# Optimization experiments

Measured on AMD Instinct MI355X. Metric: run time of the kernel, lower is better.

Reference implementation:

```python
import jax, jax.numpy as jnp
import numpy as np


def setup_inputs() -> dict:
    key = jax.random.key(0)
    k1, k2 = jax.random.split(key)
    N, C, H, W = 64, 1024, 28, 28
    x = jax.random.normal(k1, (N, C, H, W), dtype=jnp.float32)
    fc_weights = jax.random.normal(k2, (C,), dtype=jnp.float32)
    mu = jnp.float32(0.7)
    return {"x": x, "fc_weights": fc_weights, "mu": mu}


def reference(x, fc_weights, mu):
    # cams = relu(x * w_c), shape [N, C, H, W]
    cams = jax.nn.relu(x * fc_weights.reshape(1, -1, 1, 1))
    # per-(sample, channel) spatial max -> threshold
    cam_max = jnp.max(cams, axis=(2, 3), keepdims=True)        # [N, C, 1, 1]
    thr = cam_max * mu
    # drop (zero out) high-activation regions, keep the rest
    dropped = jnp.where(cams > thr, jnp.zeros_like(cams), cams)
    # accumulate over channels -> [N, 1, H, W]
    mean_drop_cam = jnp.sum(dropped, axis=1, keepdims=True)
    return x * mean_drop_cam
```

## Files before the change

### kernel.cpp

```cpp
#include <hip/hip_runtime.h>

#define HWD 784
#define Q4  196
#define CD  1024
#define ND  64

#define CHPB 32
#define NCHUNK (CD / CHPB)

typedef float f32x4 __attribute__((ext_vector_type(4)));

__device__ __forceinline__ float4 cam4(float4 v, float wc) {
    float4 r;
    r.x = fmaxf(v.x * wc, 0.f);
    r.y = fmaxf(v.y * wc, 0.f);
    r.z = fmaxf(v.z * wc, 0.f);
    r.w = fmaxf(v.w * wc, 0.f);
    return r;
}
__device__ __forceinline__ float max4(float4 v) {
    return fmaxf(fmaxf(v.x, v.y), fmaxf(v.z, v.w));
}
__device__ __forceinline__ void accdrop(float4& a, float4 c, float thr) {
    a.x += (c.x > thr) ? 0.f : c.x;
    a.y += (c.y > thr) ? 0.f : c.y;
    a.z += (c.z > thr) ? 0.f : c.z;
    a.w += (c.w > thr) ? 0.f : c.w;
}

__global__ void __launch_bounds__(256) pass1_kernel(const float* __restrict__ x,
                                                    const float* __restrict__ w,
                                                    const float* __restrict__ mu_p,
                                                    float* __restrict__ Spart) {
    __shared__ float4 drp[4][197];

    const int t = threadIdx.x;
    const int wave = t >> 6;
    const int lane = t & 63;
    const int n = blockIdx.y;
    const int cbase = blockIdx.x * CHPB + wave * 8;
    const float mu = mu_p[0];

    const float4* rows = reinterpret_cast<const float4*>(x + ((size_t)n * CD + cbase) * HWD);

    float4 acc0 = {0.f,0.f,0.f,0.f}, acc1 = {0.f,0.f,0.f,0.f};
    float4 acc2 = {0.f,0.f,0.f,0.f}, acc3 = {0.f,0.f,0.f,0.f};

    #pragma unroll 1
    for (int j = 0; j < 8; ++j) {
        const float4* r = rows + j * Q4;
        float4 v0 = r[lane];
        float4 v1 = r[lane + 64];
        float4 v2 = r[lane + 128];
        float4 v3 = (lane < 4) ? r[192 + lane] : float4{0.f,0.f,0.f,0.f};
        const float wc = w[cbase + j];

        v0 = cam4(v0, wc); v1 = cam4(v1, wc); v2 = cam4(v2, wc); v3 = cam4(v3, wc);

        float m = fmaxf(fmaxf(max4(v0), max4(v1)), fmaxf(max4(v2), max4(v3)));
        #pragma unroll
        for (int off = 32; off > 0; off >>= 1)
            m = fmaxf(m, __shfl_xor(m, off, 64));
        const float thr = m * mu;

        accdrop(acc0, v0, thr);
        accdrop(acc1, v1, thr);
        accdrop(acc2, v2, thr);
        accdrop(acc3, v3, thr);
    }

    drp[wave][lane]       = acc0;
    drp[wave][64 + lane]  = acc1;
    drp[wave][128 + lane] = acc2;
    if (lane < 4) drp[wave][192 + lane] = acc3;
    __syncthreads();

    const float* f = reinterpret_cast<const float*>(&drp[0][0]);
    float* sp = Spart + ((size_t)blockIdx.x * ND + n) * HWD;
    for (int p = t; p < HWD; p += 256)
        sp[p] = f[p] + f[788 + p] + f[2 * 788 + p] + f[3 * 788 + p];
}

__global__ void __launch_bounds__(256) reduce_kernel(const float* __restrict__ Spart,
                                                     float* __restrict__ S) {
    const int j = blockIdx.x * 256 + threadIdx.x;
    float s = 0.f;
    #pragma unroll
    for (int ch = 0; ch < NCHUNK; ++ch)
        s += Spart[(size_t)ch * ND * HWD + j];
    S[j] = s;
}

__global__ void __launch_bounds__(256) mult_kernel(const float* __restrict__ x,
                                                   const float* __restrict__ S,
                                                   float* __restrict__ out) {
    const float4* x4 = reinterpret_cast<const float4*>(x);
    const float4* S4 = reinterpret_cast<const float4*>(S);

    const int tid = blockIdx.x * 256 + threadIdx.x;
    const int n   = tid / (64 * Q4);
    const int rem = tid - n * (64 * Q4);
    const int c0  = rem / Q4;
    const int p4  = rem - c0 * Q4;

    const float4 sv = S4[n * Q4 + p4];
    size_t i4 = ((size_t)(n * CD + c0)) * Q4 + p4;

    #pragma unroll 4
    for (int k = 0; k < 16; ++k, i4 += (size_t)64 * Q4) {
        float4 xv = x4[i4];
        float4 o;
        o.x = xv.x * sv.x;
        o.y = xv.y * sv.y;
        o.z = xv.z * sv.z;
        o.w = xv.w * sv.w;
        __builtin_nontemporal_store(*reinterpret_cast<const f32x4*>(&o),
                                    reinterpret_cast<f32x4*>(out) + i4);
    }
}

extern "C" void kernel_launch(void* const* d_in, const int* in_sizes, int n_in,
                              void* d_out, int out_size, void* d_ws, size_t ws_size,
                              hipStream_t stream) {
    const float* x  = (const float*)d_in[0];
    const float* w  = (const float*)d_in[1];
    const float* mu = (const float*)d_in[2];
    float* out = (float*)d_out;

    float* Spart = (float*)d_ws;
    float* S     = Spart + (size_t)NCHUNK * ND * HWD;

    dim3 g1(NCHUNK, ND);
    pass1_kernel<<<g1, 256, 0, stream>>>(x, w, mu, Spart);

    reduce_kernel<<<ND * HWD / 256, 256, 0, stream>>>(Spart, S);

    mult_kernel<<<3136, 256, 0, stream>>>(x, S, out);
}
```

Before: 98.89 us.

## Drop in-block LDS reduction and write per-wave channel partials to workspace

The first pass now uses 128-thread blocks where each wave owns a channel chunk and stores its partial drop-sum straight to global memory, removing the shared-memory reduction and the barrier. The number of chunks is picked at runtime: 128 when the workspace is large enough, otherwise 32. The reduce kernel now loops over this runtime chunk count. With 128 chunks the partial buffer grows fourfold, which adds global write and read traffic. The reduce kernel also has to do a longer serial sum over only a few hundred blocks.

```diff
diff --git a/kernel.cpp b/kernel.cpp
--- a/kernel.cpp
+++ b/kernel.cpp
@@ -4,9 +4,6 @@
 #define Q4  196
 #define CD  1024
 #define ND  64
-
-#define CHPB 32
-#define NCHUNK (CD / CHPB)
 
 typedef float f32x4 __attribute__((ext_vector_type(4)));
 
@@ -28,17 +25,17 @@
     a.w += (c.w > thr) ? 0.f : c.w;
 }
 
-__global__ void __launch_bounds__(256) pass1_kernel(const float* __restrict__ x,
+__global__ void __launch_bounds__(128) pass1_kernel(const float* __restrict__ x,
                                                     const float* __restrict__ w,
                                                     const float* __restrict__ mu_p,
-                                                    float* __restrict__ Spart) {
-    __shared__ float4 drp[4][197];
-
+                                                    float* __restrict__ Spart,
+                                                    int cpw) {
     const int t = threadIdx.x;
     const int wave = t >> 6;
     const int lane = t & 63;
     const int n = blockIdx.y;
-    const int cbase = blockIdx.x * CHPB + wave * 8;
+    const int chunk = blockIdx.x * 2 + wave;
+    const int cbase = chunk * cpw;
     const float mu = mu_p[0];
 
     const float4* rows = reinterpret_cast<const float4*>(x + ((size_t)n * CD + cbase) * HWD);
@@ -47,7 +44,7 @@
     float4 acc2 = {0.f,0.f,0.f,0.f}, acc3 = {0.f,0.f,0.f,0.f};
 
     #pragma unroll 1
-    for (int j = 0; j < 8; ++j) {
+    for (int j = 0; j < cpw; ++j) {
         const float4* r = rows + j * Q4;
         float4 v0 = r[lane];
         float4 v1 = r[lane + 64];
@@ -69,24 +66,19 @@
         accdrop(acc3, v3, thr);
     }
 
-    drp[wave][lane]       = acc0;
-    drp[wave][64 + lane]  = acc1;
-    drp[wave][128 + lane] = acc2;
-    if (lane < 4) drp[wave][192 + lane] = acc3;
-    __syncthreads();
-
-    const float* f = reinterpret_cast<const float*>(&drp[0][0]);
-    float* sp = Spart + ((size_t)blockIdx.x * ND + n) * HWD;
-    for (int p = t; p < HWD; p += 256)
-        sp[p] = f[p] + f[788 + p] + f[2 * 788 + p] + f[3 * 788 + p];
+    float4* sp4 = reinterpret_cast<float4*>(Spart + ((size_t)chunk * ND + n) * HWD);
+    sp4[lane]        = acc0;
+    sp4[64 + lane]   = acc1;
+    sp4[128 + lane]  = acc2;
+    if (lane < 4) sp4[192 + lane] = acc3;
 }
 
 __global__ void __launch_bounds__(256) reduce_kernel(const float* __restrict__ Spart,
-                                                     float* __restrict__ S) {
+                                                     float* __restrict__ S,
+                                                     int nchunk) {
     const int j = blockIdx.x * 256 + threadIdx.x;
     float s = 0.f;
-    #pragma unroll
-    for (int ch = 0; ch < NCHUNK; ++ch)
+    for (int ch = 0; ch < nchunk; ++ch)
         s += Spart[(size_t)ch * ND * HWD + j];
     S[j] = s;
 }
@@ -127,13 +119,17 @@
     const float* mu = (const float*)d_in[2];
     float* out = (float*)d_out;
 
+    const size_t row = (size_t)ND * HWD;
+    int nchunk = (ws_size >= (128 + 1) * row * sizeof(float)) ? 128 : 32;
+    const int cpw = CD / nchunk;
+
     float* Spart = (float*)d_ws;
-    float* S     = Spart + (size_t)NCHUNK * ND * HWD;
+    float* S     = Spart + (size_t)nchunk * row;
 
-    dim3 g1(NCHUNK, ND);
-    pass1_kernel<<<g1, 256, 0, stream>>>(x, w, mu, Spart);
+    dim3 g1(nchunk / 2, ND);
+    pass1_kernel<<<g1, 128, 0, stream>>>(x, w, mu, Spart, cpw);
 
-    reduce_kernel<<<ND * HWD / 256, 256, 0, stream>>>(Spart, S);
+    reduce_kernel<<<ND * HWD / 256, 256, 0, stream>>>(Spart, S, nchunk);
 
     mult_kernel<<<3136, 256, 0, stream>>>(x, S, out);
 }
```

After: 131.2 us. +32.7%, slower.

## Stage pass1 input rows into LDS via async global_load_lds with smaller channel chunks

Applied to the files above, without the earlier changes.

Pass1 now uses 16 channels per block. It issues all of its row loads up front with direct global-to-LDS loads, waits at a barrier, and then computes from LDS, so every block has many loads in flight. The grid is flattened, with the sample index as the fast-varying part of the block id. The 50KB LDS buffer is reused for the partial-sum reduction. The price is more Spart partials (64 chunks), which doubles the reduce kernel's traffic, and lower occupancy from the larger LDS footprint. Unroll factors in the reduce and multiply kernels are also adjusted.

```diff
diff --git a/kernel.cpp b/kernel.cpp
--- a/kernel.cpp
+++ b/kernel.cpp
@@ -5,10 +5,12 @@
 #define CD  1024
 #define ND  64
 
-#define CHPB 32
+#define CHPB 16
 #define NCHUNK (CD / CHPB)
 
 typedef float f32x4 __attribute__((ext_vector_type(4)));
+typedef const __attribute__((address_space(1))) void* gas_t;
+typedef __attribute__((address_space(3))) void* las_t;
 
 __device__ __forceinline__ float4 cam4(float4 v, float wc) {
     float4 r;
@@ -32,28 +34,45 @@
                                                     const float* __restrict__ w,
                                                     const float* __restrict__ mu_p,
                                                     float* __restrict__ Spart) {
-    __shared__ float4 drp[4][197];
+    __shared__ float lds[CHPB][HWD];
 
     const int t = threadIdx.x;
     const int wave = t >> 6;
     const int lane = t & 63;
-    const int n = blockIdx.y;
-    const int cbase = blockIdx.x * CHPB + wave * 8;
+    const int n = blockIdx.x & (ND - 1);
+    const int chunk = blockIdx.x >> 6;
+    const int cbase = chunk * CHPB;
     const float mu = mu_p[0];
 
-    const float4* rows = reinterpret_cast<const float4*>(x + ((size_t)n * CD + cbase) * HWD);
+    const float* xbase = x + ((size_t)n * CD + cbase) * HWD;
+    #pragma unroll
+    for (int j = 0; j < 4; ++j) {
+        const int r = wave * 4 + j;
+        const float* rowg = xbase + (size_t)r * HWD;
+        #pragma unroll
+        for (int k = 0; k < 3; ++k) {
+            __builtin_amdgcn_global_load_lds((gas_t)(rowg + k * 256 + lane * 4),
+                                             (las_t)&lds[r][k * 256], 16, 0, 0);
+        }
+        if (lane < 4) {
+            __builtin_amdgcn_global_load_lds((gas_t)(rowg + 768 + lane * 4),
+                                             (las_t)&lds[r][768], 16, 0, 0);
+        }
+    }
+    __syncthreads();
 
     float4 acc0 = {0.f,0.f,0.f,0.f}, acc1 = {0.f,0.f,0.f,0.f};
     float4 acc2 = {0.f,0.f,0.f,0.f}, acc3 = {0.f,0.f,0.f,0.f};
 
-    #pragma unroll 1
-    for (int j = 0; j < 8; ++j) {
-        const float4* r = rows + j * Q4;
-        float4 v0 = r[lane];
-        float4 v1 = r[lane + 64];
-        float4 v2 = r[lane + 128];
-        float4 v3 = (lane < 4) ? r[192 + lane] : float4{0.f,0.f,0.f,0.f};
-        const float wc = w[cbase + j];
+    #pragma unroll
+    for (int j = 0; j < 4; ++j) {
+        const int r = wave * 4 + j;
+        float4 v0 = *reinterpret_cast<const float4*>(&lds[r][4 * lane]);
+        float4 v1 = *reinterpret_cast<const float4*>(&lds[r][256 + 4 * lane]);
+        float4 v2 = *reinterpret_cast<const float4*>(&lds[r][512 + 4 * lane]);
+        float4 v3 = (lane < 4) ? *reinterpret_cast<const float4*>(&lds[r][768 + 4 * lane])
+                               : float4{0.f,0.f,0.f,0.f};
+        const float wc = w[cbase + r];
 
         v0 = cam4(v0, wc); v1 = cam4(v1, wc); v2 = cam4(v2, wc); v3 = cam4(v3, wc);
 
@@ -69,14 +88,17 @@
         accdrop(acc3, v3, thr);
     }
 
-    drp[wave][lane]       = acc0;
-    drp[wave][64 + lane]  = acc1;
-    drp[wave][128 + lane] = acc2;
-    if (lane < 4) drp[wave][192 + lane] = acc3;
     __syncthreads();
 
-    const float* f = reinterpret_cast<const float*>(&drp[0][0]);
-    float* sp = Spart + ((size_t)blockIdx.x * ND + n) * HWD;
+    float* f = &lds[0][0];
+    float4* drp4 = reinterpret_cast<float4*>(f);
+    drp4[wave * 197 + lane]       = acc0;
+    drp4[wave * 197 + 64 + lane]  = acc1;
+    drp4[wave * 197 + 128 + lane] = acc2;
+    if (lane < 4) drp4[wave * 197 + 192 + lane] = acc3;
+    __syncthreads();
+
+    float* sp = Spart + ((size_t)chunk * ND + n) * HWD;
     for (int p = t; p < HWD; p += 256)
         sp[p] = f[p] + f[788 + p] + f[2 * 788 + p] + f[3 * 788 + p];
 }
@@ -85,7 +107,7 @@
                                                      float* __restrict__ S) {
     const int j = blockIdx.x * 256 + threadIdx.x;
     float s = 0.f;
-    #pragma unroll
+    #pragma unroll 8
     for (int ch = 0; ch < NCHUNK; ++ch)
         s += Spart[(size_t)ch * ND * HWD + j];
     S[j] = s;
@@ -106,7 +128,7 @@
     const float4 sv = S4[n * Q4 + p4];
     size_t i4 = ((size_t)(n * CD + c0)) * Q4 + p4;
 
-    #pragma unroll 4
+    #pragma unroll 8
     for (int k = 0; k < 16; ++k, i4 += (size_t)64 * Q4) {
         float4 xv = x4[i4];
         float4 o;
@@ -130,8 +152,7 @@
     float* Spart = (float*)d_ws;
     float* S     = Spart + (size_t)NCHUNK * ND * HWD;
 
-    dim3 g1(NCHUNK, ND);
-    pass1_kernel<<<g1, 256, 0, stream>>>(x, w, mu, Spart);
+    pass1_kernel<<<NCHUNK * ND, 256, 0, stream>>>(x, w, mu, Spart);
 
     reduce_kernel<<<ND * HWD / 256, 256, 0, stream>>>(Spart, S);
 
```

After: 109.9 us. +11.1%, slower.
